# Optimization experiments

Hardware: AMD Instinct MI355X
Metric: run time of the kernel (lower is better)

## Reference

```python
import jax, jax.numpy as jnp
import numpy as np
from jax import lax

SMOOTHING = 0.3
B, T, D = 64, 4096, 256


def setup_inputs() -> dict:
    key = jax.random.key(0)
    x = jax.random.normal(key, (B, T, D), dtype=jnp.float32)
    return {"x": x}


def reference(x) -> jnp.ndarray:
    # EMA linear recurrence: y[0] = x[0]; y[t] = s*x[t] + (1-s)*y[t-1]
    # Expressed as y[t] = a[t]*y[t-1] + b[t] and solved with an associative scan.
    s = jnp.asarray(SMOOTHING, x.dtype)
    t = x.shape[1]
    # a: (1, T, 1) broadcastable coefficient; a[0]=0 so y[0]=b[0]=x[0]
    a = jnp.full((1, t, 1), 1.0 - s, dtype=x.dtype).at[:, 0].set(0.0)
    b = (s * x).at[:, 0].set(x[:, 0])

    def combine(c1, c2):
        a1, b1 = c1
        a2, b2 = c2
        return a1 * a2, a2 * b1 + b2

    _, y = lax.associative_scan(combine, (a, b), axis=1)
    return y
```

## Files before the change

kernel.cpp:

```cpp
#include <hip/hip_runtime.h>


typedef float f32x4 __attribute__((ext_vector_type(4)));

constexpr int   Bc = 64;
constexpr int   Tc = 4096;
constexpr int   Dc = 256;
constexpr float S  = 0.3f;
constexpr float R  = 1.0f - S;

constexpr int L  = 128;
constexpr int W  = 32;
constexpr int DQ = Dc / 4;
constexpr int NC = Tc / L;

__global__ __launch_bounds__(256)
void ema_f32_kernel(const f32x4* __restrict__ x,
                    f32x4* __restrict__ y)
{
    const int cpx = gridDim.x >> 3;
    const int lb  = (blockIdx.x & 7) * cpx + (blockIdx.x >> 3);

    const int tid = lb * 256 + (int)threadIdx.x;
    const int dq  = tid & (DQ - 1);
    const int c   = (tid >> 6) & (NC - 1);
    const int b   = tid >> 11;
    const int t0  = c * L;
    const int base = b * (Tc * DQ) + dq;

    float y0 = 0.f, y1 = 0.f, y2 = 0.f, y3 = 0.f;
    int tstart = t0;

    if (c == 0) {
        f32x4 v = x[base];
        y0 = v.x; y1 = v.y; y2 = v.z; y3 = v.w;
        __builtin_nontemporal_store(v, &y[base]);
        tstart = 1;
    } else {
        #pragma unroll 8
        for (int t = t0 - W; t < t0; ++t) {
            f32x4 v = x[base + t * DQ];
            y0 = fmaf(R, y0, S * v.x);
            y1 = fmaf(R, y1, S * v.y);
            y2 = fmaf(R, y2, S * v.z);
            y3 = fmaf(R, y3, S * v.w);
        }
    }

    #pragma unroll 8
    for (int t = tstart; t < t0 + L; ++t) {
        f32x4 v = x[base + t * DQ];
        y0 = fmaf(R, y0, S * v.x);
        y1 = fmaf(R, y1, S * v.y);
        y2 = fmaf(R, y2, S * v.z);
        y3 = fmaf(R, y3, S * v.w);
        f32x4 o;
        o.x = y0; o.y = y1; o.z = y2; o.w = y3;
        __builtin_nontemporal_store(o, &y[base + t * DQ]);
    }
}

extern "C" void kernel_launch(void* const* d_in, const int* in_sizes, int n_in,
                              void* d_out, int out_size, void* d_ws, size_t ws_size,
                              hipStream_t stream) {
    (void)in_sizes; (void)n_in; (void)d_ws; (void)ws_size; (void)out_size;
    const f32x4* x = (const f32x4*)d_in[0];
    f32x4*       y = (f32x4*)d_out;

    const int total_threads = Bc * NC * DQ;
    dim3 grid(total_threads / 256), block(256);
    hipLaunchKernelGGL(ema_f32_kernel, grid, block, 0, stream, x, y);
}
```

Before: 452.9 us.

## Halve chunk length, shorten warmup, and double-buffer loads in registers

Chunks shrink from 128 to 64 timesteps, doubling the number of threads, and the warmup window drops from 32 to 24 steps. The main loop now prefetches the next group of 8 vectors into registers while the current group is computed and stored. This aims to hide memory latency through more parallelism and more loads in flight. The cost is more redundant warmup reads relative to work, a larger truncation error from the shorter warmup, and higher register pressure.

```diff
diff --git a/kernel.cpp b/kernel.cpp
--- a/kernel.cpp
+++ b/kernel.cpp
@@ -9,37 +9,38 @@
 constexpr float S  = 0.3f;
 constexpr float R  = 1.0f - S;
 
-constexpr int L  = 128;
-constexpr int W  = 32;
+constexpr int L  = 64;
+constexpr int W  = 24;
 constexpr int DQ = Dc / 4;
 constexpr int NC = Tc / L;
+constexpr int G  = 8;
+constexpr int NG = L / G;
 
 __global__ __launch_bounds__(256)
 void ema_f32_kernel(const f32x4* __restrict__ x,
                     f32x4* __restrict__ y)
 {
     const int cpx = gridDim.x >> 3;
-    const int lb  = (blockIdx.x & 7) * cpx + (blockIdx.x >> 3);
+    const int lb  = ((int)blockIdx.x & 7) * cpx + ((int)blockIdx.x >> 3);
 
     const int tid = lb * 256 + (int)threadIdx.x;
     const int dq  = tid & (DQ - 1);
     const int c   = (tid >> 6) & (NC - 1);
-    const int b   = tid >> 11;
+    const int b   = tid >> 12;
     const int t0  = c * L;
     const int base = b * (Tc * DQ) + dq;
 
-    float y0 = 0.f, y1 = 0.f, y2 = 0.f, y3 = 0.f;
-    int tstart = t0;
+    float y0, y1, y2, y3;
 
     if (c == 0) {
         f32x4 v = x[base];
         y0 = v.x; y1 = v.y; y2 = v.z; y3 = v.w;
-        __builtin_nontemporal_store(v, &y[base]);
-        tstart = 1;
     } else {
-        #pragma unroll 8
-        for (int t = t0 - W; t < t0; ++t) {
-            f32x4 v = x[base + t * DQ];
+        y0 = 0.f; y1 = 0.f; y2 = 0.f; y3 = 0.f;
+        const f32x4* __restrict__ wp = x + base + (t0 - W) * DQ;
+        #pragma unroll
+        for (int t = 0; t < W; ++t) {
+            f32x4 v = wp[t * DQ];
             y0 = fmaf(R, y0, S * v.x);
             y1 = fmaf(R, y1, S * v.y);
             y2 = fmaf(R, y2, S * v.z);
@@ -47,16 +48,32 @@
         }
     }
 
-    #pragma unroll 8
-    for (int t = tstart; t < t0 + L; ++t) {
-        f32x4 v = x[base + t * DQ];
-        y0 = fmaf(R, y0, S * v.x);
-        y1 = fmaf(R, y1, S * v.y);
-        y2 = fmaf(R, y2, S * v.z);
-        y3 = fmaf(R, y3, S * v.w);
-        f32x4 o;
-        o.x = y0; o.y = y1; o.z = y2; o.w = y3;
-        __builtin_nontemporal_store(o, &y[base + t * DQ]);
+    const f32x4* __restrict__ xp = x + base + t0 * DQ;
+    f32x4*       __restrict__ yp = y + base + t0 * DQ;
+
+    f32x4 cur[G];
+    #pragma unroll
+    for (int i = 0; i < G; ++i) cur[i] = xp[i * DQ];
+
+    #pragma unroll
+    for (int g = 0; g < NG; ++g) {
+        f32x4 nxt[G];
+        if (g + 1 < NG) {
+            #pragma unroll
+            for (int i = 0; i < G; ++i) nxt[i] = xp[((g + 1) * G + i) * DQ];
+        }
+        #pragma unroll
+        for (int i = 0; i < G; ++i) {
+            y0 = fmaf(R, y0, S * cur[i].x);
+            y1 = fmaf(R, y1, S * cur[i].y);
+            y2 = fmaf(R, y2, S * cur[i].z);
+            y3 = fmaf(R, y3, S * cur[i].w);
+            f32x4 o;
+            o.x = y0; o.y = y1; o.z = y2; o.w = y3;
+            __builtin_nontemporal_store(o, &yp[(g * G + i) * DQ]);
+        }
+        #pragma unroll
+        for (int i = 0; i < G; ++i) cur[i] = nxt[i];
     }
 }
 
```

Result: no change. 449.0 us (-0.9%).
